# Optimization experiments

Hardware: AMD Instinct MI355X
Metric: run time of the kernel (lower is better)

## Reference

```python
import jax, jax.numpy as jnp
import numpy as np

B, C, T = 128, 64, 128   # batch, num_channels (EEG electrodes), EEG_SEGMENT_LENGTH
HID = 128                # hidden_dim
E = HID // 2             # attention embed dim = 64
NH = 4                   # attention heads


def setup_inputs() -> dict:
    key = jax.random.key(0)
    ks = jax.random.split(key, 12)
    s = lambda k, shp, sc: jax.random.normal(k, shp, dtype=jnp.float32) * sc
    return {
        "eeg_data": jax.random.normal(ks[0], (B, C, T), dtype=jnp.float32),
        "gcn1_w": s(ks[1], (HID, T), 0.05),   # nn.Linear(T, HID): W [out,in]
        "gcn1_b": jnp.zeros((HID,), jnp.float32),
        "gcn2_w": s(ks[2], (E, HID), 0.05),
        "gcn2_b": jnp.zeros((E,), jnp.float32),
        "bn1_g": jnp.ones((C,), jnp.float32),
        "bn1_b": jnp.zeros((C,), jnp.float32),
        "bn2_g": jnp.ones((C,), jnp.float32),
        "bn2_b": jnp.zeros((C,), jnp.float32),
        "attn_in_w": s(ks[3], (3 * E, E), 0.08),   # packed q,k,v projection
        "attn_in_b": jnp.zeros((3 * E,), jnp.float32),
        "attn_out_w": s(ks[4], (E, E), 0.08),
        "attn_out_b": jnp.zeros((E,), jnp.float32),
    }


def _hilbert_phase(x):
    # torch.fft.fft -> zero bins [n//2:] (even n) -> *2 -> ifft -> angle
    n = x.shape[-1]
    half = n // 2 if n % 2 == 0 else (n + 1) // 2
    X = jnp.fft.fft(x, axis=-1)
    mask = (jnp.arange(n) < half).astype(jnp.float32) * 2.0
    analytic = jnp.fft.ifft(X * mask, axis=-1)
    return jnp.angle(analytic)


def _wpli(eeg):
    phase = _hilbert_phase(eeg)                         # [B,C,T]
    pd = phase[:, :, None, :] - phase[:, None, :, :]    # [B,C,C,T]
    pli = jnp.abs(jnp.mean(jnp.sign(jnp.sin(pd)), axis=-1))  # [B,C,C]
    eye = jnp.eye(pli.shape[-1], dtype=pli.dtype)
    return pli * (1.0 - eye)[None]


def _gcn(x, adj, w, b):
    # D^{-1/2} A D^{-1/2} via row/col scaling (equiv to diag_embed + bmm)
    deg = jnp.sum(adj, axis=2)                          # [B,C]
    dn = 1.0 / jnp.sqrt(deg + 1e-8)
    adj_n = adj * dn[:, :, None] * dn[:, None, :]
    support = jnp.einsum('bij,bjf->bif', adj_n, x)
    return support @ w.T + b


def _bn(x, g, b):
    # BatchNorm1d over channel dim C of [B,C,F]; batch stats over (B,F)
    m = jnp.mean(x, axis=(0, 2), keepdims=True)
    v = jnp.var(x, axis=(0, 2), keepdims=True)
    return (x - m) / jnp.sqrt(v + 1e-5) * g[None, :, None] + b[None, :, None]


def _mha(x, in_w, in_b, out_w, out_b):
    bsz, n, e = x.shape
    hd = e // NH
    qkv = x @ in_w.T + in_b                             # [B,N,3E]
    q, k, v = jnp.split(qkv, 3, axis=-1)
    sp = lambda t: t.reshape(bsz, n, NH, hd).transpose(0, 2, 1, 3)  # [B,H,N,hd]
    q, k, v = sp(q), sp(k), sp(v)
    scores = jnp.einsum('bhqd,bhkd->bhqk', q, k) / jnp.sqrt(jnp.float32(hd))
    attn = jax.nn.softmax(scores, axis=-1)
    o = jnp.einsum('bhqk,bhkd->bhqd', attn, v)
    o = o.transpose(0, 2, 1, 3).reshape(bsz, n, e)
    return o @ out_w.T + out_b


def reference(eeg_data, gcn1_w, gcn1_b, gcn2_w, gcn2_b, bn1_g, bn1_b,
              bn2_g, bn2_b, attn_in_w, attn_in_b, attn_out_w, attn_out_b):
    wpli = _wpli(eeg_data)                              # [B,C,C]
    x = jax.nn.relu(_bn(_gcn(eeg_data, wpli, gcn1_w, gcn1_b), bn1_g, bn1_b))
    x = jax.nn.relu(_bn(_gcn(x, wpli, gcn2_w, gcn2_b), bn2_g, bn2_b))
    x = _mha(x, attn_in_w, attn_in_b, attn_out_w, attn_out_b)
    features = jnp.mean(x, axis=1)                      # [B, E]
    return features, wpli
```

## Files before the change

### kernel.cpp

```cpp
#include <hip/hip_runtime.h>
#include <math.h>

#define NB 128
#define NC 64
#define NT 128
#define HIDN 128
#define NE 64
#define NHD 4
#define HD 16

__global__ void analytic_kernel(const float* __restrict__ eeg,
                                float* __restrict__ re, float* __restrict__ im) {
    int row = blockIdx.x;
    int t = threadIdx.x;
    __shared__ float xs[NT];
    __shared__ double cotv[64];
    xs[t] = eeg[row * NT + t];
    if (t < 64) {
        double d = (double)(2 * t + 1);
        double a = 3.14159265358979323846 * d / 128.0;
        cotv[t] = cos(a) / sin(a);
    }
    __syncthreads();
    double ar = 0.0, ai = 0.0;
    #pragma unroll
    for (int m = 0; m < 64; ++m) {
        int d = 2 * m + 1;
        int s = (t - d) & 127;
        double xv = (double)xs[s];
        ar += xv;
        ai += cotv[m] * xv;
    }
    double rr = (double)xs[t] + ar * (1.0 / 64.0);
    double ii = ai * (1.0 / 64.0);
    re[row * NT + t] = (float)rr;
    im[row * NT + t] = (float)ii;
}

__global__ void pli_kernel(const float* __restrict__ re, const float* __restrict__ im,
                           float* __restrict__ wpli, float* __restrict__ deg) {
    int b = blockIdx.x >> 4;
    int i0 = (blockIdx.x & 15) << 2;
    int tid = threadIdx.x;
    int w = tid >> 6;
    int j = tid & 63;
    __shared__ float4 sre4[64 * 32];
    __shared__ float4 sim4[64 * 32];
    __shared__ int pacc[4][4][64];
    const float* reb = re + b * (NC * NT);
    const float* imb = im + b * (NC * NT);
    for (int idx4 = tid; idx4 < 2048; idx4 += 256) {
        int c = idx4 >> 5, t4 = idx4 & 31;
        int slot = c * 32 + (t4 ^ (c & 31));
        sre4[slot] = ((const float4*)reb)[idx4];
        sim4[slot] = ((const float4*)imb)[idx4];
    }
    __syncthreads();
    int acc0 = 0, acc1 = 0, acc2 = 0, acc3 = 0;
    #pragma unroll
    for (int tt = 0; tt < 8; ++tt) {
        int t4 = w * 8 + tt;
        float4 rj = sre4[j * 32 + (t4 ^ (j & 31))];
        float4 ij = sim4[j * 32 + (t4 ^ (j & 31))];
        #pragma unroll
        for (int di = 0; di < 4; ++di) {
            int i = i0 + di;
            float4 ri = sre4[i * 32 + (t4 ^ (i & 31))];
            float4 ii = sim4[i * 32 + (t4 ^ (i & 31))];
            float c0 = ii.x * rj.x - ri.x * ij.x;
            float c1 = ii.y * rj.y - ri.y * ij.y;
            float c2 = ii.z * rj.z - ri.z * ij.z;
            float c3 = ii.w * rj.w - ri.w * ij.w;
            int d = ((c0 > 0.f) ? 1 : ((c0 < 0.f) ? -1 : 0))
                  + ((c1 > 0.f) ? 1 : ((c1 < 0.f) ? -1 : 0))
                  + ((c2 > 0.f) ? 1 : ((c2 < 0.f) ? -1 : 0))
                  + ((c3 > 0.f) ? 1 : ((c3 < 0.f) ? -1 : 0));
            if (di == 0) acc0 += d;
            else if (di == 1) acc1 += d;
            else if (di == 2) acc2 += d;
            else acc3 += d;
        }
    }
    pacc[w][0][j] = acc0; pacc[w][1][j] = acc1;
    pacc[w][2][j] = acc2; pacc[w][3][j] = acc3;
    __syncthreads();
    int di2 = tid >> 6, j2 = tid & 63;
    int a = pacc[0][di2][j2] + pacc[1][di2][j2] + pacc[2][di2][j2] + pacc[3][di2][j2];
    float p = fabsf((float)a * (1.f / (float)NT));
    int i = i0 + di2;
    if (j2 == i) p = 0.f;
    wpli[b * (NC * NC) + i * NC + j2] = p;
    float s = p;
    #pragma unroll
    for (int off = 32; off > 0; off >>= 1) s += __shfl_down(s, off);
    if (j2 == 0) deg[b * NC + i] = s;
}

template <int OUT, bool BN_IN>
__global__ __launch_bounds__(1024, 1) void gcn_fused(
        const float* __restrict__ adj, const float* __restrict__ deg,
        const float* __restrict__ x, const double* __restrict__ dpart_in,
        const float* __restrict__ g, const float* __restrict__ bb,
        const float* __restrict__ W, const float* __restrict__ bias,
        float* __restrict__ xout, double* __restrict__ dpart_out) {
    int b = blockIdx.x >> 1;
    int half = blockIdx.x & 1;
    int tid = threadIdx.x;
    __shared__ float dn_s[64];
    __shared__ float stat_s[64][2];
    __shared__ float arow[32][68];
    __shared__ float xs[64][128];
    __shared__ float sup[32][132];
    __shared__ float WsT[128][(OUT == 128) ? 132 : 68];
    __shared__ double dred[16][64][2];

    if (BN_IN) {
        int c = tid & 63, chunk = tid >> 6;
        double s = 0.0, s2 = 0.0;
        for (int bi = chunk * 8; bi < chunk * 8 + 8; ++bi) {
            s  += dpart_in[(bi * 64 + c) * 2];
            s2 += dpart_in[(bi * 64 + c) * 2 + 1];
        }
        dred[chunk][c][0] = s;
        dred[chunk][c][1] = s2;
    }
    if (tid < 64)
        dn_s[tid] = (float)(1.0 / sqrt((double)deg[b * 64 + tid] + 1e-8));
    __syncthreads();
    if (BN_IN && tid < 64) {
        double s = 0.0, s2 = 0.0;
        for (int ch = 0; ch < 16; ++ch) {
            s  += dred[ch][tid][0];
            s2 += dred[ch][tid][1];
        }
        double N = (double)(NB * HIDN);
        double m = s / N;
        double var = s2 / N - m * m;
        stat_s[tid][0] = (float)m;
        stat_s[tid][1] = (float)(1.0 / sqrt(var + 1e-5));
    }
    __syncthreads();
    if (tid < 512) {
        int il = tid >> 4, j4 = tid & 15;
        int i = half * 32 + il;
        float4 v = *(const float4*)&adj[b * 4096 + i * 64 + j4 * 4];
        float di = dn_s[i];
        v.x *= di * dn_s[j4 * 4 + 0];
        v.y *= di * dn_s[j4 * 4 + 1];
        v.z *= di * dn_s[j4 * 4 + 2];
        v.w *= di * dn_s[j4 * 4 + 3];
        *(float4*)&arow[il][j4 * 4] = v;
    }
    #pragma unroll
    for (int p = 0; p < 2; ++p) {
        int idx4 = tid + p * 1024;
        int r = idx4 >> 5, c4 = idx4 & 31;
        float4 v = ((const float4*)(x + b * 8192))[idx4];
        if (BN_IN) {
            float m = stat_s[r][0], rs = stat_s[r][1], gg = g[r], bv = bb[r];
            v.x = (v.x - m) * rs * gg + bv; v.x = v.x > 0.f ? v.x : 0.f;
            v.y = (v.y - m) * rs * gg + bv; v.y = v.y > 0.f ? v.y : 0.f;
            v.z = (v.z - m) * rs * gg + bv; v.z = v.z > 0.f ? v.z : 0.f;
            v.w = (v.w - m) * rs * gg + bv; v.w = v.w > 0.f ? v.w : 0.f;
        }
        *(float4*)&xs[r][c4 * 4] = v;
    }
    #pragma unroll
    for (int p = 0; p < OUT / 32; ++p) {
        int idx4 = tid + p * 1024;
        int o = idx4 & (OUT - 1);
        int k4 = idx4 / OUT;
        float4 w = *(const float4*)&W[o * 128 + k4 * 4];
        WsT[k4 * 4 + 0][o] = w.x;
        WsT[k4 * 4 + 1][o] = w.y;
        WsT[k4 * 4 + 2][o] = w.z;
        WsT[k4 * 4 + 3][o] = w.w;
    }
    __syncthreads();

    int il = tid >> 5;
    int i = half * 32 + il;
    {
        int f0 = (tid & 31) * 4;
        float a0 = 0.f, a1 = 0.f, a2 = 0.f, a3 = 0.f;
        #pragma unroll 8
        for (int j = 0; j < 64; ++j) {
            float a = arow[il][j];
            float4 xv = *(const float4*)&xs[j][f0];
            a0 += a * xv.x; a1 += a * xv.y; a2 += a * xv.z; a3 += a * xv.w;
        }
        *(float4*)&sup[il][f0] = make_float4(a0, a1, a2, a3);
    }
    __syncthreads();

    double ds = 0.0, ds2 = 0.0;
    if (OUT == 128) {
        int o0 = (tid & 31) * 4;
        float c[4] = {};
        #pragma unroll 8
        for (int k = 0; k < 128; ++k) {
            float s = sup[il][k];
            float4 w0 = *(const float4*)&WsT[k][o0];
            c[0] += s * w0.x; c[1] += s * w0.y; c[2] += s * w0.z; c[3] += s * w0.w;
        }
        float4 r0 = make_float4(c[0] + bias[o0], c[1] + bias[o0 + 1],
                                c[2] + bias[o0 + 2], c[3] + bias[o0 + 3]);
        *(float4*)&xout[b * 64 * 128 + i * 128 + o0] = r0;
        ds  = (double)r0.x + (double)r0.y + (double)r0.z + (double)r0.w;
        ds2 = (double)r0.x * r0.x + (double)r0.y * r0.y
            + (double)r0.z * r0.z + (double)r0.w * r0.w;
    } else {
        int o0 = (tid & 31) * 2;
        float c0 = 0.f, c1 = 0.f;
        #pragma unroll 8
        for (int k = 0; k < 128; ++k) {
            float s = sup[il][k];
            c0 += s * WsT[k][o0];
            c1 += s * WsT[k][o0 + 1];
        }
        c0 += bias[o0];
        c1 += bias[o0 + 1];
        *(float2*)&xout[b * 64 * 64 + i * 64 + o0] = make_float2(c0, c1);
        ds  = (double)c0 + (double)c1;
        ds2 = (double)c0 * c0 + (double)c1 * c1;
    }
    #pragma unroll
    for (int off = 16; off > 0; off >>= 1) {
        ds  += __shfl_down(ds, off, 32);
        ds2 += __shfl_down(ds2, off, 32);
    }
    if ((tid & 31) == 0) {
        dpart_out[(b * 64 + i) * 2]     = ds;
        dpart_out[(b * 64 + i) * 2 + 1] = ds2;
    }
}

__global__ __launch_bounds__(256) void attn_head(
        const float* __restrict__ x2, const double* __restrict__ dpart2,
        const float* __restrict__ g, const float* __restrict__ bb,
        const float* __restrict__ Win, const float* __restrict__ bin,
        float* __restrict__ w_mo) {
    int b = blockIdx.x >> 2, h = blockIdx.x & 3;
    int tid = threadIdx.x;
    int lane = tid & 63, wv = tid >> 6;
    __shared__ double dred[4][64][2];
    __shared__ float stat_s[64][2];
    __shared__ float xs[64][68];
    __shared__ float ws[48][64];
    __shared__ float kqkv[48][64];
    __shared__ float pm_s[4][64], ps_s[4][64];
    __shared__ float pool_s[16][17];

    {
        double s = 0.0, s2 = 0.0;
        for (int bi = wv * 32; bi < wv * 32 + 32; ++bi) {
            s  += dpart2[(bi * 64 + lane) * 2];
            s2 += dpart2[(bi * 64 + lane) * 2 + 1];
        }
        dred[wv][lane][0] = s;
        dred[wv][lane][1] = s2;
    }
    __syncthreads();
    if (tid < 64) {
        double s  = dred[0][tid][0] + dred[1][tid][0] + dred[2][tid][0] + dred[3][tid][0];
        double s2 = dred[0][tid][1] + dred[1][tid][1] + dred[2][tid][1] + dred[3][tid][1];
        double N = (double)(NB * NE);
        double m = s / N;
        double var = s2 / N - m * m;
        stat_s[tid][0] = (float)m;
        stat_s[tid][1] = (float)(1.0 / sqrt(var + 1e-5));
    }
    __syncthreads();
    for (int idx4 = tid; idx4 < 1024; idx4 += 256) {
        int r = idx4 >> 4, c4 = idx4 & 15;
        float4 v = ((const float4*)(x2 + b * 4096))[idx4];
        float m = stat_s[r][0], rs = stat_s[r][1], gg = g[r], bv = bb[r];
        v.x = (v.x - m) * rs * gg + bv; v.x = v.x > 0.f ? v.x : 0.f;
        v.y = (v.y - m) * rs * gg + bv; v.y = v.y > 0.f ? v.y : 0.f;
        v.z = (v.z - m) * rs * gg + bv; v.z = v.z > 0.f ? v.z : 0.f;
        v.w = (v.w - m) * rs * gg + bv; v.w = v.w > 0.f ? v.w : 0.f;
        *(float4*)&xs[r][c4 * 4] = v;
    }
    for (int idx4 = tid; idx4 < 768; idx4 += 256) {
        int rl = idx4 >> 4, c4 = idx4 & 15;
        int rg = ((rl >> 4) << 6) + (h << 4) + (rl & 15);
        *(float4*)&ws[rl][c4 * 4] = ((const float4*)(Win + rg * 64))[c4];
    }
    __syncthreads();

    float acc[12];
    #pragma unroll
    for (int u = 0; u < 12; ++u) {
        int ol = wv + 4 * u;
        acc[u] = bin[((ol >> 4) << 6) + (h << 4) + (ol & 15)];
    }
    #pragma unroll
    for (int d4 = 0; d4 < 16; ++d4) {
        float4 xv = *(const float4*)&xs[lane][d4 * 4];
        #pragma unroll
        for (int u = 0; u < 12; ++u) {
            float4 w = *(const float4*)&ws[wv + 4 * u][d4 * 4];
            acc[u] += xv.x * w.x + xv.y * w.y + xv.z * w.z + xv.w * w.w;
        }
    }
    #pragma unroll
    for (int u = 0; u < 12; ++u) kqkv[wv + 4 * u][lane] = acc[u];
    __syncthreads();

    int j0 = wv * 16;
    float q[16];
    #pragma unroll
    for (int d = 0; d < 16; ++d) q[d] = kqkv[d][lane];
    float sc[16];
    #pragma unroll
    for (int jj = 0; jj < 16; ++jj) sc[jj] = 0.f;
    #pragma unroll
    for (int d = 0; d < 16; ++d) {
        float qd = q[d];
        #pragma unroll
        for (int j4 = 0; j4 < 4; ++j4) {
            float4 kv = *(const float4*)&kqkv[16 + d][j0 + j4 * 4];
            sc[j4 * 4 + 0] += qd * kv.x;
            sc[j4 * 4 + 1] += qd * kv.y;
            sc[j4 * 4 + 2] += qd * kv.z;
            sc[j4 * 4 + 3] += qd * kv.w;
        }
    }
    float pmax = -1e30f;
    #pragma unroll
    for (int jj = 0; jj < 16; ++jj) { sc[jj] *= 0.25f; pmax = fmaxf(pmax, sc[jj]); }
    pm_s[wv][lane] = pmax;
    __syncthreads();
    float mx = fmaxf(fmaxf(pm_s[0][lane], pm_s[1][lane]),
                     fmaxf(pm_s[2][lane], pm_s[3][lane]));
    float psum = 0.f;
    #pragma unroll
    for (int jj = 0; jj < 16; ++jj) { sc[jj] = expf(sc[jj] - mx); psum += sc[jj]; }
    ps_s[wv][lane] = psum;
    float po[16];
    #pragma unroll
    for (int d = 0; d < 16; ++d) {
        float4 v0 = *(const float4*)&kqkv[32 + d][j0 + 0];
        float4 v1 = *(const float4*)&kqkv[32 + d][j0 + 4];
        float4 v2 = *(const float4*)&kqkv[32 + d][j0 + 8];
        float4 v3 = *(const float4*)&kqkv[32 + d][j0 + 12];
        po[d] = sc[0] * v0.x + sc[1] * v0.y + sc[2] * v0.z + sc[3] * v0.w
              + sc[4] * v1.x + sc[5] * v1.y + sc[6] * v1.z + sc[7] * v1.w
              + sc[8] * v2.x + sc[9] * v2.y + sc[10] * v2.z + sc[11] * v2.w
              + sc[12] * v3.x + sc[13] * v3.y + sc[14] * v3.z + sc[15] * v3.w;
    }
    __syncthreads();
    float inv = 1.f / (ps_s[0][lane] + ps_s[1][lane] + ps_s[2][lane] + ps_s[3][lane]);
    if (wv == 0) {
        #pragma unroll
        for (int d = 0; d < 16; ++d) kqkv[d][lane] = po[d];
    }
    __syncthreads();
    if (wv == 1) {
        #pragma unroll
        for (int d = 0; d < 16; ++d) kqkv[d][lane] += po[d];
    }
    __syncthreads();
    if (wv == 2) {
        #pragma unroll
        for (int d = 0; d < 16; ++d) kqkv[d][lane] += po[d];
    }
    __syncthreads();
    if (wv == 3) {
        #pragma unroll
        for (int d = 0; d < 16; ++d)
            kqkv[d][lane] = (kqkv[d][lane] + po[d]) * inv;
    }
    __syncthreads();
    {
        int d = tid & 15, part = tid >> 4;
        float4 v = *(const float4*)&kqkv[d][part * 4];
        pool_s[d][part] = v.x + v.y + v.z + v.w;
    }
    __syncthreads();
    if (tid < 16) {
        float s = 0.f;
        #pragma unroll
        for (int p = 0; p < 16; ++p) s += pool_s[tid][p];
        w_mo[b * 64 + h * 16 + tid] = s * (1.f / 64.f);
    }
}

__global__ void proj_kernel(const float* __restrict__ w_mo,
                            const float* __restrict__ Wout,
                            const float* __restrict__ bout,
                            float* __restrict__ feat) {
    int b = blockIdx.x;
    int tid = threadIdx.x;
    __shared__ float mos[64];
    mos[tid] = w_mo[b * 64 + tid];
    __syncthreads();
    float acc = bout[tid];
    const float4* wr = (const float4*)(Wout + tid * 64);
    #pragma unroll
    for (int d4 = 0; d4 < 16; ++d4) {
        float4 w = wr[d4];
        acc += mos[d4 * 4 + 0] * w.x + mos[d4 * 4 + 1] * w.y
             + mos[d4 * 4 + 2] * w.z + mos[d4 * 4 + 3] * w.w;
    }
    feat[b * NE + tid] = acc;
}

extern "C" void kernel_launch(void* const* d_in, const int* in_sizes, int n_in,
                              void* d_out, int out_size, void* d_ws, size_t ws_size,
                              hipStream_t stream) {
    const float* eeg      = (const float*)d_in[0];
    const float* gcn1_w   = (const float*)d_in[1];
    const float* gcn1_b   = (const float*)d_in[2];
    const float* gcn2_w   = (const float*)d_in[3];
    const float* gcn2_b   = (const float*)d_in[4];
    const float* bn1_g    = (const float*)d_in[5];
    const float* bn1_b    = (const float*)d_in[6];
    const float* bn2_g    = (const float*)d_in[7];
    const float* bn2_b    = (const float*)d_in[8];
    const float* attn_in_w  = (const float*)d_in[9];
    const float* attn_in_b  = (const float*)d_in[10];
    const float* attn_out_w = (const float*)d_in[11];
    const float* attn_out_b = (const float*)d_in[12];

    float* out  = (float*)d_out;
    float* feat = out;
    float* wpli = out + NB * NE;

    float* ws = (float*)d_ws;
    float*  w_re   = ws;
    float*  w_im   = ws + 1048576;
    float*  w_x1   = ws + 2097152;
    float*  w_x2   = ws + 3145728;
    float*  w_deg  = ws + 3670016;
    float*  w_mo   = ws + 3678208;
    double* dpart1 = (double*)(ws + 3686400);
    double* dpart2 = (double*)(ws + 3719168);

    analytic_kernel<<<NB * NC, NT, 0, stream>>>(eeg, w_re, w_im);
    pli_kernel<<<NB * NC / 4, 256, 0, stream>>>(w_re, w_im, wpli, w_deg);
    gcn_fused<HIDN, false><<<NB * 2, 1024, 0, stream>>>(
        wpli, w_deg, eeg, nullptr, nullptr, nullptr,
        gcn1_w, gcn1_b, w_x1, dpart1);
    gcn_fused<NE, true><<<NB * 2, 1024, 0, stream>>>(
        wpli, w_deg, w_x1, dpart1, bn1_g, bn1_b,
        gcn2_w, gcn2_b, w_x2, dpart2);
    attn_head<<<NB * NHD, 256, 0, stream>>>(w_x2, dpart2, bn2_g, bn2_b,
                                            attn_in_w, attn_in_b, w_mo);
    proj_kernel<<<NB, NE, 0, stream>>>(w_mo, attn_out_w, attn_out_b, feat);
}
```

Before: 98.73 us.

## Fuse both GCN layers with a grid barrier and fold projection into attention

Merges the two GCN launches into one persistent kernel. A software grid-wide barrier separates layer 1 from layer 2 so the BatchNorm statistics are complete before layer 2 reads them. The output projection kernel is removed: the last attention-head block for each batch, found with an atomic counter, computes it. This cuts two kernel launches and reuses the normalized adjacency rows kept in shared memory, but adds a memset launch and depends on all 256 blocks being resident at once for the barrier to avoid deadlock.

```diff
diff --git a/kernel.cpp b/kernel.cpp
--- a/kernel.cpp
+++ b/kernel.cpp
@@ -96,13 +96,27 @@
     if (j2 == 0) deg[b * NC + i] = s;
 }
 
-template <int OUT, bool BN_IN>
-__global__ __launch_bounds__(1024, 1) void gcn_fused(
+__device__ __forceinline__ void grid_bar(int* bar, int nblk) {
+    __threadfence();
+    __syncthreads();
+    if (threadIdx.x == 0) {
+        __hip_atomic_fetch_add(bar, 1, __ATOMIC_ACQ_REL, __HIP_MEMORY_SCOPE_AGENT);
+        while (__hip_atomic_load(bar, __ATOMIC_ACQUIRE, __HIP_MEMORY_SCOPE_AGENT) < nblk)
+            __builtin_amdgcn_s_sleep(8);
+    }
+    __syncthreads();
+    __threadfence();
+}
+
+__global__ __launch_bounds__(1024, 1) void gcn12(
         const float* __restrict__ adj, const float* __restrict__ deg,
-        const float* __restrict__ x, const double* __restrict__ dpart_in,
-        const float* __restrict__ g, const float* __restrict__ bb,
-        const float* __restrict__ W, const float* __restrict__ bias,
-        float* __restrict__ xout, double* __restrict__ dpart_out) {
+        const float* __restrict__ eeg,
+        const float* __restrict__ g1w, const float* __restrict__ g1b,
+        const float* __restrict__ g2w, const float* __restrict__ g2b,
+        const float* __restrict__ bn1g, const float* __restrict__ bn1b,
+        float* __restrict__ w_x1, float* __restrict__ w_x2,
+        double* __restrict__ dpart1, double* __restrict__ dpart2,
+        int* __restrict__ bar) {
     int b = blockIdx.x >> 1;
     int half = blockIdx.x & 1;
     int tid = threadIdx.x;
@@ -111,34 +125,11 @@
     __shared__ float arow[32][68];
     __shared__ float xs[64][128];
     __shared__ float sup[32][132];
-    __shared__ float WsT[128][(OUT == 128) ? 132 : 68];
+    __shared__ float WsT[128][132];
     __shared__ double dred[16][64][2];
 
-    if (BN_IN) {
-        int c = tid & 63, chunk = tid >> 6;
-        double s = 0.0, s2 = 0.0;
-        for (int bi = chunk * 8; bi < chunk * 8 + 8; ++bi) {
-            s  += dpart_in[(bi * 64 + c) * 2];
-            s2 += dpart_in[(bi * 64 + c) * 2 + 1];
-        }
-        dred[chunk][c][0] = s;
-        dred[chunk][c][1] = s2;
-    }
     if (tid < 64)
         dn_s[tid] = (float)(1.0 / sqrt((double)deg[b * 64 + tid] + 1e-8));
-    __syncthreads();
-    if (BN_IN && tid < 64) {
-        double s = 0.0, s2 = 0.0;
-        for (int ch = 0; ch < 16; ++ch) {
-            s  += dred[ch][tid][0];
-            s2 += dred[ch][tid][1];
-        }
-        double N = (double)(NB * HIDN);
-        double m = s / N;
-        double var = s2 / N - m * m;
-        stat_s[tid][0] = (float)m;
-        stat_s[tid][1] = (float)(1.0 / sqrt(var + 1e-5));
-    }
     __syncthreads();
     if (tid < 512) {
         int il = tid >> 4, j4 = tid & 15;
@@ -155,29 +146,20 @@
     for (int p = 0; p < 2; ++p) {
         int idx4 = tid + p * 1024;
         int r = idx4 >> 5, c4 = idx4 & 31;
-        float4 v = ((const float4*)(x + b * 8192))[idx4];
-        if (BN_IN) {
-            float m = stat_s[r][0], rs = stat_s[r][1], gg = g[r], bv = bb[r];
-            v.x = (v.x - m) * rs * gg + bv; v.x = v.x > 0.f ? v.x : 0.f;
-            v.y = (v.y - m) * rs * gg + bv; v.y = v.y > 0.f ? v.y : 0.f;
-            v.z = (v.z - m) * rs * gg + bv; v.z = v.z > 0.f ? v.z : 0.f;
-            v.w = (v.w - m) * rs * gg + bv; v.w = v.w > 0.f ? v.w : 0.f;
-        }
+        float4 v = ((const float4*)(eeg + b * 8192))[idx4];
         *(float4*)&xs[r][c4 * 4] = v;
     }
     #pragma unroll
-    for (int p = 0; p < OUT / 32; ++p) {
+    for (int p = 0; p < 4; ++p) {
         int idx4 = tid + p * 1024;
-        int o = idx4 & (OUT - 1);
-        int k4 = idx4 / OUT;
-        float4 w = *(const float4*)&W[o * 128 + k4 * 4];
+        int o = idx4 & 127, k4 = idx4 >> 7;
+        float4 w = *(const float4*)&g1w[o * 128 + k4 * 4];
         WsT[k4 * 4 + 0][o] = w.x;
         WsT[k4 * 4 + 1][o] = w.y;
         WsT[k4 * 4 + 2][o] = w.z;
         WsT[k4 * 4 + 3][o] = w.w;
     }
     __syncthreads();
-
     int il = tid >> 5;
     int i = half * 32 + il;
     {
@@ -192,9 +174,7 @@
         *(float4*)&sup[il][f0] = make_float4(a0, a1, a2, a3);
     }
     __syncthreads();
-
-    double ds = 0.0, ds2 = 0.0;
-    if (OUT == 128) {
+    {
         int o0 = (tid & 31) * 4;
         float c[4] = {};
         #pragma unroll 8
@@ -203,13 +183,83 @@
             float4 w0 = *(const float4*)&WsT[k][o0];
             c[0] += s * w0.x; c[1] += s * w0.y; c[2] += s * w0.z; c[3] += s * w0.w;
         }
-        float4 r0 = make_float4(c[0] + bias[o0], c[1] + bias[o0 + 1],
-                                c[2] + bias[o0 + 2], c[3] + bias[o0 + 3]);
-        *(float4*)&xout[b * 64 * 128 + i * 128 + o0] = r0;
-        ds  = (double)r0.x + (double)r0.y + (double)r0.z + (double)r0.w;
-        ds2 = (double)r0.x * r0.x + (double)r0.y * r0.y
-            + (double)r0.z * r0.z + (double)r0.w * r0.w;
-    } else {
+        float4 r0 = make_float4(c[0] + g1b[o0], c[1] + g1b[o0 + 1],
+                                c[2] + g1b[o0 + 2], c[3] + g1b[o0 + 3]);
+        *(float4*)&w_x1[b * 8192 + i * 128 + o0] = r0;
+        double ds  = (double)r0.x + (double)r0.y + (double)r0.z + (double)r0.w;
+        double ds2 = (double)r0.x * r0.x + (double)r0.y * r0.y
+                   + (double)r0.z * r0.z + (double)r0.w * r0.w;
+        #pragma unroll
+        for (int off = 16; off > 0; off >>= 1) {
+            ds  += __shfl_down(ds, off, 32);
+            ds2 += __shfl_down(ds2, off, 32);
+        }
+        if ((tid & 31) == 0) {
+            dpart1[(b * 64 + i) * 2]     = ds;
+            dpart1[(b * 64 + i) * 2 + 1] = ds2;
+        }
+    }
+    grid_bar(bar, NB * 2);
+    {
+        int c = tid & 63, chunk = tid >> 6;
+        double s = 0.0, s2 = 0.0;
+        for (int bi = chunk * 8; bi < chunk * 8 + 8; ++bi) {
+            s  += dpart1[(bi * 64 + c) * 2];
+            s2 += dpart1[(bi * 64 + c) * 2 + 1];
+        }
+        dred[chunk][c][0] = s;
+        dred[chunk][c][1] = s2;
+    }
+    __syncthreads();
+    if (tid < 64) {
+        double s = 0.0, s2 = 0.0;
+        for (int ch = 0; ch < 16; ++ch) {
+            s  += dred[ch][tid][0];
+            s2 += dred[ch][tid][1];
+        }
+        double N = (double)(NB * HIDN);
+        double m = s / N;
+        double var = s2 / N - m * m;
+        stat_s[tid][0] = (float)m;
+        stat_s[tid][1] = (float)(1.0 / sqrt(var + 1e-5));
+    }
+    __syncthreads();
+    #pragma unroll
+    for (int p = 0; p < 2; ++p) {
+        int idx4 = tid + p * 1024;
+        int r = idx4 >> 5, c4 = idx4 & 31;
+        float4 v = ((const float4*)(w_x1 + b * 8192))[idx4];
+        float m = stat_s[r][0], rs = stat_s[r][1], gg = bn1g[r], bv = bn1b[r];
+        v.x = (v.x - m) * rs * gg + bv; v.x = v.x > 0.f ? v.x : 0.f;
+        v.y = (v.y - m) * rs * gg + bv; v.y = v.y > 0.f ? v.y : 0.f;
+        v.z = (v.z - m) * rs * gg + bv; v.z = v.z > 0.f ? v.z : 0.f;
+        v.w = (v.w - m) * rs * gg + bv; v.w = v.w > 0.f ? v.w : 0.f;
+        *(float4*)&xs[r][c4 * 4] = v;
+    }
+    #pragma unroll
+    for (int p = 0; p < 2; ++p) {
+        int idx4 = tid + p * 1024;
+        int o = idx4 & 63, k4 = idx4 >> 6;
+        float4 w = *(const float4*)&g2w[o * 128 + k4 * 4];
+        WsT[k4 * 4 + 0][o] = w.x;
+        WsT[k4 * 4 + 1][o] = w.y;
+        WsT[k4 * 4 + 2][o] = w.z;
+        WsT[k4 * 4 + 3][o] = w.w;
+    }
+    __syncthreads();
+    {
+        int f0 = (tid & 31) * 4;
+        float a0 = 0.f, a1 = 0.f, a2 = 0.f, a3 = 0.f;
+        #pragma unroll 8
+        for (int j = 0; j < 64; ++j) {
+            float a = arow[il][j];
+            float4 xv = *(const float4*)&xs[j][f0];
+            a0 += a * xv.x; a1 += a * xv.y; a2 += a * xv.z; a3 += a * xv.w;
+        }
+        *(float4*)&sup[il][f0] = make_float4(a0, a1, a2, a3);
+    }
+    __syncthreads();
+    {
         int o0 = (tid & 31) * 2;
         float c0 = 0.f, c1 = 0.f;
         #pragma unroll 8
@@ -218,20 +268,20 @@
             c0 += s * WsT[k][o0];
             c1 += s * WsT[k][o0 + 1];
         }
-        c0 += bias[o0];
-        c1 += bias[o0 + 1];
-        *(float2*)&xout[b * 64 * 64 + i * 64 + o0] = make_float2(c0, c1);
-        ds  = (double)c0 + (double)c1;
-        ds2 = (double)c0 * c0 + (double)c1 * c1;
-    }
-    #pragma unroll
-    for (int off = 16; off > 0; off >>= 1) {
-        ds  += __shfl_down(ds, off, 32);
-        ds2 += __shfl_down(ds2, off, 32);
-    }
-    if ((tid & 31) == 0) {
-        dpart_out[(b * 64 + i) * 2]     = ds;
-        dpart_out[(b * 64 + i) * 2 + 1] = ds2;
+        c0 += g2b[o0];
+        c1 += g2b[o0 + 1];
+        *(float2*)&w_x2[b * 4096 + i * 64 + o0] = make_float2(c0, c1);
+        double ds  = (double)c0 + (double)c1;
+        double ds2 = (double)c0 * c0 + (double)c1 * c1;
+        #pragma unroll
+        for (int off = 16; off > 0; off >>= 1) {
+            ds  += __shfl_down(ds, off, 32);
+            ds2 += __shfl_down(ds2, off, 32);
+        }
+        if ((tid & 31) == 0) {
+            dpart2[(b * 64 + i) * 2]     = ds;
+            dpart2[(b * 64 + i) * 2 + 1] = ds2;
+        }
     }
 }
 
@@ -239,7 +289,9 @@
         const float* __restrict__ x2, const double* __restrict__ dpart2,
         const float* __restrict__ g, const float* __restrict__ bb,
         const float* __restrict__ Win, const float* __restrict__ bin,
-        float* __restrict__ w_mo) {
+        const float* __restrict__ Wout, const float* __restrict__ bout,
+        float* __restrict__ w_mo, int* __restrict__ cnt,
+        float* __restrict__ feat) {
     int b = blockIdx.x >> 2, h = blockIdx.x & 3;
     int tid = threadIdx.x;
     int lane = tid & 63, wv = tid >> 6;
@@ -250,6 +302,8 @@
     __shared__ float kqkv[48][64];
     __shared__ float pm_s[4][64], ps_s[4][64];
     __shared__ float pool_s[16][17];
+    __shared__ float mos[64];
+    __shared__ int last_s;
 
     {
         double s = 0.0, s2 = 0.0;
@@ -384,26 +438,30 @@
         for (int p = 0; p < 16; ++p) s += pool_s[tid][p];
         w_mo[b * 64 + h * 16 + tid] = s * (1.f / 64.f);
     }
-}
-
-__global__ void proj_kernel(const float* __restrict__ w_mo,
-                            const float* __restrict__ Wout,
-                            const float* __restrict__ bout,
-                            float* __restrict__ feat) {
-    int b = blockIdx.x;
-    int tid = threadIdx.x;
-    __shared__ float mos[64];
-    mos[tid] = w_mo[b * 64 + tid];
-    __syncthreads();
-    float acc = bout[tid];
-    const float4* wr = (const float4*)(Wout + tid * 64);
-    #pragma unroll
-    for (int d4 = 0; d4 < 16; ++d4) {
-        float4 w = wr[d4];
-        acc += mos[d4 * 4 + 0] * w.x + mos[d4 * 4 + 1] * w.y
-             + mos[d4 * 4 + 2] * w.z + mos[d4 * 4 + 3] * w.w;
-    }
-    feat[b * NE + tid] = acc;
+    __syncthreads();
+    if (tid == 0) {
+        __threadfence();
+        int old = __hip_atomic_fetch_add(&cnt[b], 1, __ATOMIC_ACQ_REL,
+                                         __HIP_MEMORY_SCOPE_AGENT);
+        last_s = (old == 3) ? 1 : 0;
+    }
+    __syncthreads();
+    if (last_s) {
+        __threadfence();
+        if (tid < 64) mos[tid] = w_mo[b * 64 + tid];
+        __syncthreads();
+        if (tid < 64) {
+            float a = bout[tid];
+            const float4* wr = (const float4*)(Wout + tid * 64);
+            #pragma unroll
+            for (int d4 = 0; d4 < 16; ++d4) {
+                float4 w = wr[d4];
+                a += mos[d4 * 4 + 0] * w.x + mos[d4 * 4 + 1] * w.y
+                   + mos[d4 * 4 + 2] * w.z + mos[d4 * 4 + 3] * w.w;
+            }
+            feat[b * NE + tid] = a;
+        }
+    }
 }
 
 extern "C" void kernel_launch(void* const* d_in, const int* in_sizes, int n_in,
@@ -436,16 +494,16 @@
     float*  w_mo   = ws + 3678208;
     double* dpart1 = (double*)(ws + 3686400);
     double* dpart2 = (double*)(ws + 3719168);
-
+    int*    sync_i = (int*)(ws + 3751936);
+
+    hipMemsetAsync(sync_i, 0, 520, stream);
     analytic_kernel<<<NB * NC, NT, 0, stream>>>(eeg, w_re, w_im);
     pli_kernel<<<NB * NC / 4, 256, 0, stream>>>(w_re, w_im, wpli, w_deg);
-    gcn_fused<HIDN, false><<<NB * 2, 1024, 0, stream>>>(
-        wpli, w_deg, eeg, nullptr, nullptr, nullptr,
-        gcn1_w, gcn1_b, w_x1, dpart1);
-    gcn_fused<NE, true><<<NB * 2, 1024, 0, stream>>>(
-        wpli, w_deg, w_x1, dpart1, bn1_g, bn1_b,
-        gcn2_w, gcn2_b, w_x2, dpart2);
+    gcn12<<<NB * 2, 1024, 0, stream>>>(
+        wpli, w_deg, eeg, gcn1_w, gcn1_b, gcn2_w, gcn2_b,
+        bn1_g, bn1_b, w_x1, w_x2, dpart1, dpart2, sync_i);
     attn_head<<<NB * NHD, 256, 0, stream>>>(w_x2, dpart2, bn2_g, bn2_b,
-                                            attn_in_w, attn_in_b, w_mo);
-    proj_kernel<<<NB, NE, 0, stream>>>(w_mo, attn_out_w, attn_out_b, feat);
+                                            attn_in_w, attn_in_b,
+                                            attn_out_w, attn_out_b,
+                                            w_mo, sync_i + 2, feat);
 }
```

After: 287.8 us. 192% more time.
